# Optimization experiments

Measured on AMD Instinct MI355X. Metric: run time of the kernel, lower is better.

Reference implementation:

```python
import jax, jax.numpy as jnp
import numpy as np

T = 2048   # block_size
V = 1024   # vocab_size
B = 8


def setup_inputs() -> dict:
    key = jax.random.key(0)
    k_idx, k_v = jax.random.split(key)
    idx = jax.random.randint(k_idx, (B, T), 0, V, dtype=jnp.int64 if jax.config.jax_enable_x64 else jnp.int32)
    # nn.Embedding(4,1) init: normal(mean=0, std=0.02) (the constant init is overwritten)
    v_weight = jax.random.normal(k_v, (4, 1), dtype=jnp.float32) * 0.02
    return {"idx": idx, "v_weight": v_weight}


def reference(idx, v_weight):
    # one-hot token 'embedding': [B, T, V]
    e = jax.nn.one_hot(idx, V, dtype=jnp.float32)

    # relative position table: pos[i,j] = i-j, clamped: <0 -> 3 (padding), >2 -> 2
    r = jnp.arange(T)
    d = r[:, None] - r[None, :]
    pidx = jnp.where(d < 0, 3, jnp.minimum(d, 2))            # [T, T] int

    tril = jnp.tril(jnp.ones((T, T), dtype=jnp.float32))     # lower-triangular mask

    # pos_embd = v(pos).squeeze().tril()
    pos_embd = v_weight[pidx, 0] * tril                      # [T, T]

    # layer_one = pos_embd @ e  -> [B, T, V]
    layer_one = jnp.einsum('ts,bsv->btv', pos_embd, e)

    # attention = e @ layer_one^T -> [B, T, T], then tril mask
    attention = jnp.einsum('btv,bsv->bts', e, layer_one)
    masked_attention = attention * tril                      # broadcast over batch

    # output = masked_attention @ e -> [B, T, V]
    logits = jnp.einsum('bts,bsv->btv', masked_attention, e)

    return jax.nn.softmax(logits, axis=-1)
```

## Files before the change

kernel.cpp:

```cpp
#include <hip/hip_runtime.h>

#define TT   2048
#define VV   1024
#define BB   8
#define ROCC 32

#define SEGP_OFF 0
#define TOT_OFF  (1u << 20)
#define OCC_OFF  ((1u << 20) + (1u << 15))

__global__ __launch_bounds__(1024) void k_setup(const int* __restrict__ idx,
                                                float* __restrict__ SEGP,
                                                float* __restrict__ TOT,
                                                int* __restrict__ OCC) {
    __shared__ unsigned int hist[16][VV];
    const int b = blockIdx.x, tid = threadIdx.x;
    const int lane = tid & 63, w = tid >> 6;
    const int* __restrict__ row = idx + b * TT;

    unsigned run = 0;
    for (int pass = 0; pass < 2; ++pass) {
        #pragma unroll
        for (int j = 0; j < 16; ++j) hist[j][tid] = 0u;
        __syncthreads();

        const int g   = pass * 16 + w;
        const int s   = (g << 6) + lane;
        const int tok = row[s];
        atomicAdd(&hist[w][tok], 1u);
        __syncthreads();

        #pragma unroll
        for (int j = 0; j < 16; ++j) {
            const unsigned h = hist[j][tid];
            hist[j][tid] = run;
            SEGP[((size_t)b * 32 + pass * 16 + j) * VV + tid] = (float)run;
            run += h;
        }
        __syncthreads();

        int cnt = 0;
        for (int i = 0; i < 64; ++i) {
            const int xi = __shfl(tok, i, 64);
            cnt += (i < lane && xi == tok) ? 1 : 0;
        }
        const int rank0 = (int)hist[w][tok] + cnt;
        if (rank0 < ROCC) OCC[((size_t)b * VV + tok) * ROCC + rank0] = s;
        __syncthreads();
    }
    TOT[b * VV + tid] = (float)run;
}

__global__ __launch_bounds__(256) void k_chain(const int* __restrict__ idx,
                                               const float* __restrict__ wt,
                                               const float* __restrict__ SEGP,
                                               const float* __restrict__ TOT,
                                               const int* __restrict__ OCC,
                                               float* __restrict__ out) {
    __shared__ float slab[4][VV];
    const int tid = threadIdx.x, lane = tid & 63, wid = tid >> 6;
    const int gw = blockIdx.x * 4 + wid;
    const int b = gw >> 10, c = gw & (VV - 1);

    const int K0 = (int)TOT[b * VV + c];
    if (K0 == 0) return;
    const int K = (K0 < ROCC) ? K0 : ROCC;

    const float w2 = wt[2], dw1 = wt[1] - w2;
    const float wself = wt[0];
    const int* __restrict__ row = idx + b * TT;
    const float* __restrict__ segp_b = SEGP + (size_t)b * 32 * VV;
    const int* __restrict__ occ = OCC + ((size_t)b * VV + c) * ROCC;

    float* __restrict__ lg = slab[wid];
    #pragma unroll
    for (int q = 0; q < 16; ++q) lg[q * 64 + lane] = 0.0f;

    float A[16], Bg[16];
    #pragma unroll
    for (int q = 0; q < 16; ++q) { A[q] = 0.0f; Bg[q] = 0.0f; }

    const int cq = c >> 6, cl = c & 63;

    for (int j = 1; j <= K; ++j) {
        const int u = occ[j - 1];
        const int g = u >> 6, r = u & 63;

        if (lane < r) atomicAdd(&lg[row[(g << 6) + lane]], 1.0f);

        float D[16];
        const float* __restrict__ pr = segp_b + (size_t)g * VV;
        #pragma unroll
        for (int q = 0; q < 16; ++q) D[q] = pr[q * 64 + lane];

        asm volatile("s_waitcnt lgkmcnt(0)" ::: "memory");
        #pragma unroll
        for (int q = 0; q < 16; ++q) {
            D[q] += lg[q * 64 + lane];
            lg[q * 64 + lane] = 0.0f;
        }

        const float jf = (float)j;
        float lo[16];
        #pragma unroll
        for (int q = 0; q < 16; ++q)
            lo[q] = w2 * (jf * D[q] - (A[q] + D[q])) + dw1 * Bg[q];
        #pragma unroll
        for (int q = 0; q < 16; ++q)
            lo[q] += (q == cq && lane == cl) ? wself * jf : 0.0f;

        #pragma unroll
        for (int q = 0; q < 16; ++q) A[q] += D[q];
        if (j < K && u + 1 < TT) {
            const int xn = row[u + 1];
            const int xq = xn >> 6, xl = xn & 63;
            #pragma unroll
            for (int q = 0; q < 16; ++q)
                Bg[q] += (q == xq && lane == xl) ? 1.0f : 0.0f;
        }

        float m = -1e30f;
        #pragma unroll
        for (int q = 0; q < 16; ++q) m = fmaxf(m, lo[q]);
        #pragma unroll
        for (int o = 32; o > 0; o >>= 1) m = fmaxf(m, __shfl_xor(m, o, 64));
        float sm = 0.0f;
        #pragma unroll
        for (int q = 0; q < 16; ++q) { lo[q] = __expf(lo[q] - m); sm += lo[q]; }
        #pragma unroll
        for (int o = 32; o > 0; o >>= 1) sm += __shfl_xor(sm, o, 64);
        const float inv = 1.0f / sm;

        float* __restrict__ op = out + ((size_t)(b * TT + u) << 10);
        #pragma unroll
        for (int q = 0; q < 16; ++q) op[q * 64 + lane] = lo[q] * inv;
    }
}

extern "C" void kernel_launch(void* const* d_in, const int* in_sizes, int n_in,
                              void* d_out, int out_size, void* d_ws, size_t ws_size,
                              hipStream_t stream) {
    const int*   idx = (const int*)d_in[0];
    const float* w   = (const float*)d_in[1];
    float*       out = (float*)d_out;
    char* ws = (char*)d_ws;
    float* SEGP = (float*)(ws + SEGP_OFF);
    float* TOT  = (float*)(ws + TOT_OFF);
    int*   OCC  = (int*)(ws + OCC_OFF);

    k_setup<<<BB, 1024, 0, stream>>>(idx, SEGP, TOT, OCC);
    k_chain<<<(BB * VV) / 4, 256, 0, stream>>>(idx, w, SEGP, TOT, OCC, out);
}
```

Before: 103.6 us.

## Prefetch next occurrence data and preload occurrence list into lanes

Loads the whole occurrence list and successor tokens into per-lane registers once, then uses shuffles instead of dependent global loads inside the chain loop. The segment-prefix row and token row for the next iteration are software-prefetched one step ahead to hide global-load latency. Output stores become nontemporal so the write stream does not pollute cache. Costs extra registers for the double-buffered 16-element arrays, which may lower occupancy.

```diff
diff --git a/kernel.cpp b/kernel.cpp
--- a/kernel.cpp
+++ b/kernel.cpp
@@ -72,6 +72,9 @@
     const float* __restrict__ segp_b = SEGP + (size_t)b * 32 * VV;
     const int* __restrict__ occ = OCC + ((size_t)b * VV + c) * ROCC;
 
+    const int myocc  = (lane < K) ? occ[lane] : 0;
+    const int mysucc = (lane < K - 1) ? row[myocc + 1] : 0;
+
     float* __restrict__ lg = slab[wid];
     #pragma unroll
     for (int q = 0; q < 16; ++q) lg[q * 64 + lane] = 0.0f;
@@ -82,21 +85,33 @@
 
     const int cq = c >> 6, cl = c & 63;
 
+    int u_cur = __shfl(myocc, 0, 64);
+    int tok_cur = row[(u_cur & ~63) + lane];
+    float Dg[16];
+    {
+        const float* __restrict__ pr = segp_b + (size_t)(u_cur >> 6) * VV;
+        #pragma unroll
+        for (int q = 0; q < 16; ++q) Dg[q] = pr[q * 64 + lane];
+    }
+
     for (int j = 1; j <= K; ++j) {
-        const int u = occ[j - 1];
-        const int g = u >> 6, r = u & 63;
+        int u_nxt = 0, tok_nxt = 0;
+        float Dg_n[16];
+        if (j < K) {
+            u_nxt = __shfl(myocc, j, 64);
+            tok_nxt = row[(u_nxt & ~63) + lane];
+            const float* __restrict__ pr = segp_b + (size_t)(u_nxt >> 6) * VV;
+            #pragma unroll
+            for (int q = 0; q < 16; ++q) Dg_n[q] = pr[q * 64 + lane];
+        }
 
-        if (lane < r) atomicAdd(&lg[row[(g << 6) + lane]], 1.0f);
+        if (lane < (u_cur & 63)) atomicAdd(&lg[tok_cur], 1.0f);
+        asm volatile("s_waitcnt lgkmcnt(0)" ::: "memory");
 
         float D[16];
-        const float* __restrict__ pr = segp_b + (size_t)g * VV;
-        #pragma unroll
-        for (int q = 0; q < 16; ++q) D[q] = pr[q * 64 + lane];
-
-        asm volatile("s_waitcnt lgkmcnt(0)" ::: "memory");
         #pragma unroll
         for (int q = 0; q < 16; ++q) {
-            D[q] += lg[q * 64 + lane];
+            D[q] = Dg[q] + lg[q * 64 + lane];
             lg[q * 64 + lane] = 0.0f;
         }
 
@@ -111,8 +126,8 @@
 
         #pragma unroll
         for (int q = 0; q < 16; ++q) A[q] += D[q];
-        if (j < K && u + 1 < TT) {
-            const int xn = row[u + 1];
+        if (j < K) {
+            const int xn = __shfl(mysucc, j - 1, 64);
             const int xq = xn >> 6, xl = xn & 63;
             #pragma unroll
             for (int q = 0; q < 16; ++q)
@@ -131,9 +146,14 @@
         for (int o = 32; o > 0; o >>= 1) sm += __shfl_xor(sm, o, 64);
         const float inv = 1.0f / sm;
 
-        float* __restrict__ op = out + ((size_t)(b * TT + u) << 10);
+        float* __restrict__ op = out + ((size_t)(b * TT + u_cur) << 10);
         #pragma unroll
-        for (int q = 0; q < 16; ++q) op[q * 64 + lane] = lo[q] * inv;
+        for (int q = 0; q < 16; ++q)
+            __builtin_nontemporal_store(lo[q] * inv, &op[q * 64 + lane]);
+
+        u_cur = u_nxt; tok_cur = tok_nxt;
+        #pragma unroll
+        for (int q = 0; q < 16; ++q) Dg[q] = Dg_n[q];
     }
 }
 
```

New measurement: 106.8 us. +3.0%, slower.

## Split each token chain across two waves with interleaved softmax output

Applied to the files above, without the earlier changes.

Each (batch, token) chain is now handled by two waves. Both waves recompute the prefix accumulators, and each one computes softmax and writes output only for every other occurrence, halving the per-wave output work at the cost of duplicated prefix work. Occurrence positions and successor tokens are preloaded once per wave and fetched with shuffles instead of per-iteration global loads. Output stores become nontemporal. The launch grid doubles.

```diff
diff --git a/kernel.cpp b/kernel.cpp
--- a/kernel.cpp
+++ b/kernel.cpp
@@ -1,9 +1,10 @@
 #include <hip/hip_runtime.h>
 
-#define TT   2048
-#define VV   1024
-#define BB   8
-#define ROCC 32
+#define TT    2048
+#define VV    1024
+#define BB    8
+#define ROCC  32
+#define SPLIT 2
 
 #define SEGP_OFF 0
 #define TOT_OFF  (1u << 20)
@@ -60,17 +61,22 @@
     __shared__ float slab[4][VV];
     const int tid = threadIdx.x, lane = tid & 63, wid = tid >> 6;
     const int gw = blockIdx.x * 4 + wid;
-    const int b = gw >> 10, c = gw & (VV - 1);
+    const int r  = gw & (SPLIT - 1);
+    const int cc = gw >> (SPLIT >> 1);
+    const int b  = cc >> 10, c = cc & (VV - 1);
 
     const int K0 = (int)TOT[b * VV + c];
-    if (K0 == 0) return;
-    const int K = (K0 < ROCC) ? K0 : ROCC;
+    const int K  = (K0 < ROCC) ? K0 : ROCC;
+    if (r >= K) return;
 
     const float w2 = wt[2], dw1 = wt[1] - w2;
     const float wself = wt[0];
     const int* __restrict__ row = idx + b * TT;
     const float* __restrict__ segp_b = SEGP + (size_t)b * 32 * VV;
     const int* __restrict__ occ = OCC + ((size_t)b * VV + c) * ROCC;
+
+    const int myocc  = (lane < K) ? occ[lane] : 0;
+    const int mysucc = (lane < K - 1) ? row[myocc + 1] : 0;
 
     float* __restrict__ lg = slab[wid];
     #pragma unroll
@@ -83,10 +89,11 @@
     const int cq = c >> 6, cl = c & 63;
 
     for (int j = 1; j <= K; ++j) {
-        const int u = occ[j - 1];
-        const int g = u >> 6, r = u & 63;
+        const int u = __shfl(myocc, j - 1, 64);
+        const int g = u >> 6, rpos = u & 63;
 
-        if (lane < r) atomicAdd(&lg[row[(g << 6) + lane]], 1.0f);
+        const int tok = row[(g << 6) + lane];
+        if (lane < rpos) atomicAdd(&lg[tok], 1.0f);
 
         float D[16];
         const float* __restrict__ pr = segp_b + (size_t)g * VV;
@@ -98,42 +105,44 @@
         for (int q = 0; q < 16; ++q) {
             D[q] += lg[q * 64 + lane];
             lg[q * 64 + lane] = 0.0f;
+            A[q] += D[q];
         }
 
-        const float jf = (float)j;
-        float lo[16];
-        #pragma unroll
-        for (int q = 0; q < 16; ++q)
-            lo[q] = w2 * (jf * D[q] - (A[q] + D[q])) + dw1 * Bg[q];
-        #pragma unroll
-        for (int q = 0; q < 16; ++q)
-            lo[q] += (q == cq && lane == cl) ? wself * jf : 0.0f;
+        if (((j - 1) & (SPLIT - 1)) == r) {
+            const float jf = (float)j;
+            float lo[16];
+            #pragma unroll
+            for (int q = 0; q < 16; ++q)
+                lo[q] = w2 * (jf * D[q] - A[q]) + dw1 * Bg[q];
+            #pragma unroll
+            for (int q = 0; q < 16; ++q)
+                lo[q] += (q == cq && lane == cl) ? wself * jf : 0.0f;
 
-        #pragma unroll
-        for (int q = 0; q < 16; ++q) A[q] += D[q];
-        if (j < K && u + 1 < TT) {
-            const int xn = row[u + 1];
+            float m = -1e30f;
+            #pragma unroll
+            for (int q = 0; q < 16; ++q) m = fmaxf(m, lo[q]);
+            #pragma unroll
+            for (int o = 32; o > 0; o >>= 1) m = fmaxf(m, __shfl_xor(m, o, 64));
+            float sm = 0.0f;
+            #pragma unroll
+            for (int q = 0; q < 16; ++q) { lo[q] = __expf(lo[q] - m); sm += lo[q]; }
+            #pragma unroll
+            for (int o = 32; o > 0; o >>= 1) sm += __shfl_xor(sm, o, 64);
+            const float inv = 1.0f / sm;
+
+            float* __restrict__ op = out + ((size_t)(b * TT + u) << 10);
+            #pragma unroll
+            for (int q = 0; q < 16; ++q)
+                __builtin_nontemporal_store(lo[q] * inv, &op[q * 64 + lane]);
+        }
+
+        if (j < K) {
+            const int xn = __shfl(mysucc, j - 1, 64);
             const int xq = xn >> 6, xl = xn & 63;
             #pragma unroll
             for (int q = 0; q < 16; ++q)
                 Bg[q] += (q == xq && lane == xl) ? 1.0f : 0.0f;
         }
-
-        float m = -1e30f;
-        #pragma unroll
-        for (int q = 0; q < 16; ++q) m = fmaxf(m, lo[q]);
-        #pragma unroll
-        for (int o = 32; o > 0; o >>= 1) m = fmaxf(m, __shfl_xor(m, o, 64));
-        float sm = 0.0f;
-        #pragma unroll
-        for (int q = 0; q < 16; ++q) { lo[q] = __expf(lo[q] - m); sm += lo[q]; }
-        #pragma unroll
-        for (int o = 32; o > 0; o >>= 1) sm += __shfl_xor(sm, o, 64);
-        const float inv = 1.0f / sm;
-
-        float* __restrict__ op = out + ((size_t)(b * TT + u) << 10);
-        #pragma unroll
-        for (int q = 0; q < 16; ++q) op[q * 64 + lane] = lo[q] * inv;
     }
 }
 
@@ -149,5 +158,5 @@
     int*   OCC  = (int*)(ws + OCC_OFF);
 
     k_setup<<<BB, 1024, 0, stream>>>(idx, SEGP, TOT, OCC);
-    k_chain<<<(BB * VV) / 4, 256, 0, stream>>>(idx, w, SEGP, TOT, OCC, out);
+    k_chain<<<(BB * VV * SPLIT) / 4, 256, 0, stream>>>(idx, w, SEGP, TOT, OCC, out);
 }
```

Result: no change. 103.9 us (+0.3%).
